# Performance work log

Measured on AMD Instinct MI355X. Metric: run time of the kernel, lower is better.

The kernel has to match this reference:

```python
import jax, jax.numpy as jnp
import numpy as np

N = 20000      # nodes
E = 300000     # edges
HID = 128
HEADS = 4
DH = HID // HEADS
NF = 4         # node_features
EF = 3         # edge_features
NS = 10        # num_servers (Q-head output)
NL = 4         # num_layers


def _ln(h, g, b):
    m = h.mean(-1, keepdims=True)
    v = ((h - m) ** 2).mean(-1, keepdims=True)
    return (h - m) / jnp.sqrt(v + 1e-5) * g + b


def _lrelu(h):
    return jnp.where(h >= 0, h, 0.2 * h)


def setup_inputs() -> dict:
    key = jax.random.key(0)
    ks = jax.random.split(key, 48)
    it = iter(range(48))

    def W(shape, fan_in):
        return jax.random.normal(ks[next(it)], shape, jnp.float32) / np.float32(np.sqrt(fan_in))

    inp = {}
    inp["x"] = jax.random.normal(ks[next(it)], (N, NF), jnp.float32)
    inp["edge_index"] = jax.random.randint(ks[next(it)], (2, E), 0, N)
    inp["edge_attr"] = jax.random.normal(ks[next(it)], (E, EF), jnp.float32)
    # node / edge encoders
    inp["ne_w"] = W((NF, HID), NF); inp["ne_b"] = jnp.zeros((HID,), jnp.float32)
    inp["ne_g"] = jnp.ones((HID,), jnp.float32); inp["ne_beta"] = jnp.zeros((HID,), jnp.float32)
    inp["ee_w"] = W((EF, HID), EF); inp["ee_b"] = jnp.zeros((HID,), jnp.float32)
    inp["ee_g"] = jnp.ones((HID,), jnp.float32); inp["ee_beta"] = jnp.zeros((HID,), jnp.float32)
    # EdgeConv layers (stacked over NL)
    inp["ec_w1"] = W((NL, 2 * HID, HID), 2 * HID); inp["ec_b1"] = jnp.zeros((NL, HID), jnp.float32)
    inp["ec_lng"] = jnp.ones((NL, HID), jnp.float32); inp["ec_lnb"] = jnp.zeros((NL, HID), jnp.float32)
    inp["ec_w2"] = W((NL, HID, HID), HID); inp["ec_b2"] = jnp.zeros((NL, HID), jnp.float32)
    inp["ec_wa"] = W((NL, 2 * HID, 1), 2 * HID); inp["ec_ba"] = jnp.zeros((NL, 1), jnp.float32)
    # GATConv layers
    inp["gat_w"] = W((NL, HID, HID), HID)
    inp["gat_asrc"] = W((NL, HEADS, DH), DH)
    inp["gat_adst"] = W((NL, HEADS, DH), DH)
    inp["gat_bias"] = jnp.zeros((NL, HID), jnp.float32)
    # post-block layer norms
    inp["ln_g"] = jnp.ones((NL, HID), jnp.float32); inp["ln_b"] = jnp.zeros((NL, HID), jnp.float32)
    # dueling heads
    inp["adv_w1"] = W((HID, HID), HID); inp["adv_b1"] = jnp.zeros((HID,), jnp.float32)
    inp["adv_g"] = jnp.ones((HID,), jnp.float32); inp["adv_beta"] = jnp.zeros((HID,), jnp.float32)
    inp["adv_w2"] = W((HID, NS), HID); inp["adv_b2"] = jnp.zeros((NS,), jnp.float32)
    inp["val_w1"] = W((HID, HID), HID); inp["val_b1"] = jnp.zeros((HID,), jnp.float32)
    inp["val_g"] = jnp.ones((HID,), jnp.float32); inp["val_beta"] = jnp.zeros((HID,), jnp.float32)
    inp["val_w2"] = W((HID, 1), HID); inp["val_b2"] = jnp.zeros((1,), jnp.float32)
    return inp


def _forward(x, edge_attr, edge_index,
             ne_w, ne_b, ne_g, ne_beta, ee_w, ee_b, ee_g, ee_beta,
             ec_w1, ec_b1, ec_lng, ec_lnb, ec_w2, ec_b2, ec_wa, ec_ba,
             gat_w, gat_asrc, gat_adst, gat_bias, ln_g, ln_b,
             adv_w1, adv_b1, adv_g, adv_beta, adv_w2, adv_b2,
             val_w1, val_b1, val_g, val_beta, val_w2, val_b2):
    src = edge_index[0]
    dst = edge_index[1]
    h = _ln(_lrelu(x @ ne_w + ne_b), ne_g, ne_beta)                 # node encoder (eval: no dropout)
    _ea = _ln(_lrelu(edge_attr @ ee_w + ee_b), ee_g, ee_beta)        # edge encoder; message() only tests presence
    deg = jax.ops.segment_sum(jnp.ones((E,), h.dtype), dst, num_segments=N)  # in-degree [N]
    sl = jnp.arange(N)
    src_sl = jnp.concatenate([src, sl])                              # GATConv adds self-loops
    dst_sl = jnp.concatenate([dst, sl])

    xc = h
    res = h
    for i in range(NL):
        # ---- EdgeConv: gather-concat, per-edge MLP, sigmoid edge-attention gate, scatter ----
        tmp = jnp.concatenate([xc[dst], xc[src]], axis=1)            # [E, 2H] = x_i || x_j
        m = _lrelu(tmp @ ec_w1[i] + ec_b1[i])
        m = _ln(m, ec_lng[i], ec_lnb[i])
        m = _lrelu(m @ ec_w2[i] + ec_b2[i])
        gate = jax.nn.sigmoid(tmp @ ec_wa[i] + ec_ba[i])             # [E, 1]
        msg = m * gate
        if i % 2 == 0:  # 'max' aggregation (PyG fills isolated nodes with 0)
            agg = jax.ops.segment_max(msg, dst, num_segments=N)
            agg = jnp.where(deg[:, None] > 0, agg, 0.0)
        else:           # 'mean'
            agg = jax.ops.segment_sum(msg, dst, num_segments=N) / jnp.maximum(deg, 1.0)[:, None]
        # ---- GATConv (self-loops, segment softmax over destination) ----
        wx = (xc @ gat_w[i]).reshape(N, HEADS, DH)
        asrc = (wx * gat_asrc[i]).sum(-1)                            # [N, HEADS]
        adst = (wx * gat_adst[i]).sum(-1)
        e = _lrelu(asrc[src_sl] + adst[dst_sl])                      # [E+N, HEADS]
        emax = jax.ops.segment_max(e, dst_sl, num_segments=N)
        p = jnp.exp(e - emax[dst_sl])
        den = jax.ops.segment_sum(p, dst_sl, num_segments=N)
        alpha = p / den[dst_sl]                                      # attention (eval: no dropout)
        gat_out = jax.ops.segment_sum(alpha[:, :, None] * wx[src_sl], dst_sl, num_segments=N)
        gat_out = gat_out.reshape(N, HID) + gat_bias[i]
        # ---- residual + norm + activation ----
        xc = _lrelu(_ln(res + agg + gat_out, ln_g[i], ln_b[i]))
        res = xc

    t = xc[0]                                                        # task node representation
    a = _ln(_lrelu(t @ adv_w1 + adv_b1), adv_g, adv_beta)
    a = a @ adv_w2 + adv_b2                                          # [NS]
    v = _ln(_lrelu(t @ val_w1 + val_b1), val_g, val_beta)
    v = v @ val_w2 + val_b2                                          # [1]
    q = v + (a - a.mean())
    return q, v


def reference(x, edge_index, edge_attr,
              ne_w, ne_b, ne_g, ne_beta, ee_w, ee_b, ee_g, ee_beta,
              ec_w1, ec_b1, ec_lng, ec_lnb, ec_w2, ec_b2, ec_wa, ec_ba,
              gat_w, gat_asrc, gat_adst, gat_bias, ln_g, ln_b,
              adv_w1, adv_b1, adv_g, adv_beta, adv_w2, adv_b2,
              val_w1, val_b1, val_g, val_beta, val_w2, val_b2):
    return _forward(x, edge_attr, edge_index,
                    ne_w, ne_b, ne_g, ne_beta, ee_w, ee_b, ee_g, ee_beta,
                    ec_w1, ec_b1, ec_lng, ec_lnb, ec_w2, ec_b2, ec_wa, ec_ba,
                    gat_w, gat_asrc, gat_adst, gat_bias, ln_g, ln_b,
                    adv_w1, adv_b1, adv_g, adv_beta, adv_w2, adv_b2,
                    val_w1, val_b1, val_g, val_beta, val_w2, val_b2)
```

## Files before the change

kernel.cpp:

```cpp
#include <hip/hip_runtime.h>
#include <hip/hip_bf16.h>

#define NN 20000
#define NE 300000
#define HIDN 128
#define NLAY 4
#define NNTILES ((NN + 63) / 64)
#define EBLOCKS64 4688
#define EB64_PER_XCD 586

typedef short short8 __attribute__((ext_vector_type(8)));
typedef float f32x4 __attribute__((ext_vector_type(4)));
typedef unsigned short us16;
typedef unsigned int u32;

__device__ __forceinline__ float lrelu(float x){ return x >= 0.f ? x : 0.2f * x; }
__device__ __forceinline__ float b2f(us16 u){ return __uint_as_float(((u32)u) << 16); }
__device__ __forceinline__ us16 f2b(float f){
    u32 u = __float_as_uint(f);
    u += 0x7FFFu + ((u >> 16) & 1u);
    return (us16)(u >> 16);
}
__device__ __forceinline__ float rawf(const void* p, size_t i, int dt){
    return dt ? b2f(((const us16*)p)[i]) : ((const float*)p)[i];
}
__device__ __forceinline__ void ld4f(const float* p, float* r){
    float4 v = *(const float4*)p; r[0]=v.x; r[1]=v.y; r[2]=v.z; r[3]=v.w;
}
__device__ __forceinline__ int swzi(int i){
    return (i & ~15) | ((i & 15) ^ (((i >> 5) & 3) << 2));
}

__device__ __forceinline__ void ln_stats_128(float v, volatile float* red, float& mean, float& inv){
    float s = v, s2 = v * v;
#pragma unroll
    for (int m = 32; m >= 1; m >>= 1){ s += __shfl_xor(s, m, 64); s2 += __shfl_xor(s2, m, 64); }
    int w = threadIdx.x >> 6;
    if ((threadIdx.x & 63) == 0){ red[w*2] = s; red[w*2+1] = s2; }
    __syncthreads();
    float ts = red[0] + red[2], ts2 = red[1] + red[3];
    mean = ts * (1.f/128.f);
    float var = ts2 * (1.f/128.f) - mean * mean;
    inv = rsqrtf(var + 1e-5f);
    __syncthreads();
}

__global__ void k_detect(const u32* __restrict__ ne_g, int* __restrict__ flag){
    flag[0] = (ne_g[0] == 0x3F803F80u) ? 1 : 0;
}

struct ConvEnt { const void* s; float* d; int n; int pad; };
struct ConvTab { ConvEnt c[28]; int cnt; int pad[3]; };

__global__ void k_convert_all(ConvTab tab, const int* __restrict__ flag){
    int ti = blockIdx.y;
    if (ti >= tab.cnt) return;
    const void* s = tab.c[ti].s;
    float* d = tab.c[ti].d;
    int n = tab.c[ti].n;
    int dt = flag[0];
    for (int i = blockIdx.x*blockDim.x + threadIdx.x; i < n; i += gridDim.x*blockDim.x)
        d[i] = rawf(s, i, dt);
}

#define W1T (128*256)
#define W2S (4*128*32)
#define GWT (128*128)
#define PER_L (W1T + W2S + GWT)
#define PTOT2 (NLAY*PER_L)
__global__ void k_prepw(const void* __restrict__ ecw1r, const void* __restrict__ ecw2r,
                        const void* __restrict__ gatwr, const int* __restrict__ flag,
                        us16* __restrict__ w1t, us16* __restrict__ w2s, us16* __restrict__ gwt){
    int id = blockIdx.x*blockDim.x + threadIdx.x;
    if (id >= PTOT2) return;
    int dt = flag[0];
    int L = id / PER_L, r = id % PER_L;
    if (r < W1T){
        int n = r >> 8, k = r & 255;
        w1t[(size_t)L*W1T + r] = f2b(rawf(ecw1r, (size_t)L*32768 + (size_t)k*128 + n, dt));
    } else if (r < W1T + W2S){
        int rr = r - W1T;
        int kk = rr >> 12, rem = rr & 4095, n = rem >> 5, ks = rem & 31;
        int k = kk*32 + ks;
        w2s[(size_t)L*W2S + rr] = f2b(rawf(ecw2r, (size_t)L*16384 + (size_t)k*128 + n, dt));
    } else {
        int rr = r - W1T - W2S; int n = rr >> 7, k = rr & 127;
        gwt[(size_t)L*GWT + rr] = f2b(rawf(gatwr, (size_t)L*16384 + (size_t)k*128 + n, dt));
    }
}

__global__ void k_hist(const int* __restrict__ dstI, int* __restrict__ cnt){
    int e = blockIdx.x*blockDim.x + threadIdx.x;
    if (e < NE) atomicAdd(&cnt[dstI[e]], 1);
}
__global__ void k_scan(const int* __restrict__ cnt, int* __restrict__ rowptr){
    __shared__ int ps[256];
    int t = threadIdx.x;
    int chunk = (NN + 255) / 256;
    int beg = t*chunk, end = beg + chunk; if (end > NN) end = NN;
    int s = 0;
    for (int i = beg; i < end; ++i) s += cnt[i];
    ps[t] = s; __syncthreads();
    int off = 0;
    for (int i = 0; i < t; ++i) off += ps[i];
    int run = off;
    for (int i = beg; i < end; ++i){ rowptr[i] = run; run += cnt[i]; }
    if (t == 255) rowptr[NN] = run;
}
__global__ void k_csrfill(const int* __restrict__ srcI, const int* __restrict__ dstI,
                          int* __restrict__ cur, int* __restrict__ csr_src,
                          int* __restrict__ csr_dst){
    int e = blockIdx.x*blockDim.x + threadIdx.x;
    if (e < NE){
        int d = dstI[e];
        int p = atomicAdd(&cur[d], 1);
        csr_src[p] = srcI[e];
        csr_dst[p] = d;
    }
}

__global__ void k_nodeenc(const float* __restrict__ xf, const float* __restrict__ w,
                          const float* __restrict__ b, const float* __restrict__ g,
                          const float* __restrict__ beta, float* __restrict__ h,
                          us16* __restrict__ xb){
    __shared__ float red[4];
    int n = blockIdx.x, t = threadIdx.x;
    float acc = b[t];
#pragma unroll
    for (int k = 0; k < 4; ++k) acc = fmaf(xf[n*4+k], w[k*HIDN+t], acc);
    acc = lrelu(acc);
    float mean, inv; ln_stats_128(acc, red, mean, inv);
    float o = (acc-mean)*inv*g[t] + beta[t];
    h[(size_t)n*HIDN+t] = o;
    xb[(size_t)n*HIDN+t] = f2b(o);
}

__global__ void k_predot(const float* __restrict__ x, const float* __restrict__ wa,
                         const float* __restrict__ baP, float* __restrict__ gd,
                         float* __restrict__ gs){
    int wv = threadIdx.x >> 6, l = threadIdx.x & 63;
    int n = blockIdx.x*4 + wv;
    if (n >= NN) return;
    float2 xv = *(const float2*)(x + (size_t)n*HIDN + 2*l);
    float pd = xv.x*wa[2*l]     + xv.y*wa[2*l+1];
    float ps = xv.x*wa[128+2*l] + xv.y*wa[129+2*l];
#pragma unroll
    for (int mk = 32; mk >= 1; mk >>= 1){ pd += __shfl_xor(pd, mk, 64); ps += __shfl_xor(ps, mk, 64); }
    if (l == 0){ gd[n] = pd + baP[0]; gs[n] = ps; }
}

__global__ __launch_bounds__(256, 2) void k_nodemm(
    const us16* __restrict__ xb, const us16* __restrict__ w1t,
    const us16* __restrict__ gwt, const float* __restrict__ b1,
    const float* __restrict__ aws, const float* __restrict__ awd,
    us16* __restrict__ y1b, us16* __restrict__ y2b, us16* __restrict__ wxb,
    float* __restrict__ asrc, float* __restrict__ adst)
{
    __shared__ __align__(16) us16 sbuf[64*128];
    int t = threadIdx.x;
    int wv = t >> 6, lane = t & 63, g = lane >> 4, lr = lane & 15;

    short8 fr[3][2][4];
#pragma unroll
    for (int m = 0; m < 3; ++m)
#pragma unroll
        for (int p = 0; p < 2; ++p){
            int crow = (wv + 4*p)*16 + lr;
#pragma unroll
            for (int kk = 0; kk < 4; ++kk){
                fr[m][p][kk] = (m < 2)
                    ? *(const short8*)(w1t + crow*256 + m*128 + kk*32 + g*8)
                    : *(const short8*)(gwt + crow*128 + kk*32 + g*8);
            }
        }
    float aw_s0 = aws[2*lane], aw_s1 = aws[2*lane+1];
    float aw_d0 = awd[2*lane], aw_d1 = awd[2*lane+1];
    float b1v[2][4];
#pragma unroll
    for (int p = 0; p < 2; ++p) ld4f(b1 + (wv + 4*p)*16 + g*4, b1v[p]);

    for (int tile = blockIdx.x; tile < NNTILES; tile += gridDim.x){
        int n0 = tile * 64;
        f32x4 acc[3][2][4];
#pragma unroll
        for (int m = 0; m < 3; ++m)
#pragma unroll
            for (int p = 0; p < 2; ++p)
#pragma unroll
                for (int et = 0; et < 4; ++et) acc[m][p][et] = (f32x4)(0.f);

#pragma unroll
        for (int et = 0; et < 4; ++et){
            int nrow = n0 + et*16 + lr; if (nrow >= NN) nrow = NN - 1;
            short8 bF[4];
#pragma unroll
            for (int kk = 0; kk < 4; ++kk)
                bF[kk] = *(const short8*)(xb + (size_t)nrow*HIDN + kk*32 + g*8);
#pragma unroll
            for (int m = 0; m < 3; ++m)
#pragma unroll
                for (int p = 0; p < 2; ++p)
#pragma unroll
                    for (int kk = 0; kk < 4; ++kk)
                        acc[m][p][et] = __builtin_amdgcn_mfma_f32_16x16x32_bf16(fr[m][p][kk], bF[kk], acc[m][p][et], 0, 0, 0);
        }

#pragma unroll
        for (int m = 0; m < 3; ++m){
#pragma unroll
            for (int p = 0; p < 2; ++p)
#pragma unroll
                for (int et = 0; et < 4; ++et){
                    int row = et*16 + lr;
                    int swz = (row & 7) << 3;
                    int c0 = (wv + 4*p)*16 + g*4;
#pragma unroll
                    for (int r = 0; r < 4; ++r){
                        float v = acc[m][p][et][r] + ((m == 0) ? b1v[p][r] : 0.f);
                        sbuf[row*128 + ((c0 + r) ^ swz)] = f2b(v);
                    }
                }
            __syncthreads();
            us16* dst = (m == 0) ? y1b : (m == 1) ? y2b : wxb;
            {
                int row = t >> 2, q = t & 3;
                int n = n0 + row;
                if (n < NN){
                    int swz = (row & 7) << 3;
#pragma unroll
                    for (int j = 0; j < 4; ++j){
                        int col = q*32 + j*8;
                        *(short8*)(dst + (size_t)n*HIDN + col) = *(const short8*)(sbuf + row*128 + (col ^ swz));
                    }
                }
            }
            if (m == 2){
#pragma unroll
                for (int i = 0; i < 16; ++i){
                    int rw = wv*16 + i;
                    int n2 = n0 + rw;
                    int ci = (2*lane) ^ ((rw & 7) << 3);
                    u32 v = *(const u32*)(sbuf + rw*128 + ci);
                    float x0 = b2f((us16)(v & 0xFFFFu)), x1 = b2f((us16)(v >> 16));
                    float ps = x0*aw_s0 + x1*aw_s1;
                    float pd = x0*aw_d0 + x1*aw_d1;
#pragma unroll
                    for (int mk = 8; mk >= 1; mk >>= 1){ ps += __shfl_xor(ps, mk, 64); pd += __shfl_xor(pd, mk, 64); }
                    if ((lane & 15) == 0 && n2 < NN){
                        int h = lane >> 4;
                        asrc[(size_t)n2*4 + h] = ps;
                        adst[(size_t)n2*4 + h] = pd;
                    }
                }
            }
            __syncthreads();
        }
    }
}

__global__ __launch_bounds__(256, 4) void k_edgeconv2(
    const us16* __restrict__ y1b, const us16* __restrict__ y2b,
    const int* __restrict__ csr_src, const int* __restrict__ csr_dst,
    const us16* __restrict__ w2s, const float* __restrict__ lngE,
    const float* __restrict__ lnbE, const float* __restrict__ b2,
    const float* __restrict__ gd, const float* __restrict__ gs,
    us16* __restrict__ msg)
{
    __shared__ __align__(16) u32 bsl[2][2048];
    __shared__ __align__(16) us16 outS[4*16*128];
    int t = threadIdx.x;
    int wv = t >> 6, lane = t & 63, g = lane >> 4, lr = lane & 15;
    int bid = (int)blockIdx.x;
    int sb = (bid & 7) * EB64_PER_XCD + (bid >> 3);
    int e0 = sb * 64;

    const u32* w2u = (const u32*)w2s;
    u32 rS[8];
#pragma unroll
    for (int q = 0; q < 8; ++q) rS[q] = w2u[t + 256*q];

    int e = e0 + wv*16 + lr;
    int ec = (e < NE) ? e : NE - 1;
    int d = csr_dst[ec], s = csr_src[ec];
    float gate = 1.f / (1.f + __expf(-(gd[d] + gs[s])));

    float vv[32];
    {
        short8 ra[4], rb[4];
#pragma unroll
        for (int kk = 0; kk < 4; ++kk){
            ra[kk] = *(const short8*)(y1b + (size_t)d*HIDN + kk*32 + g*8);
            rb[kk] = *(const short8*)(y2b + (size_t)s*HIDN + kk*32 + g*8);
        }
        float s1 = 0.f, s2 = 0.f;
#pragma unroll
        for (int kk = 0; kk < 4; ++kk)
#pragma unroll
            for (int j = 0; j < 8; ++j){
                float v = lrelu(b2f((us16)ra[kk][j]) + b2f((us16)rb[kk][j]));
                vv[kk*8+j] = v; s1 += v; s2 += v*v;
            }
        s1 += __shfl_xor(s1, 16, 64); s2 += __shfl_xor(s2, 16, 64);
        s1 += __shfl_xor(s1, 32, 64); s2 += __shfl_xor(s2, 32, 64);
        float mean = s1 * (1.f/128.f);
        float var  = s2 * (1.f/128.f) - mean*mean;
        float inv  = rsqrtf(var + 1e-5f);
#pragma unroll
        for (int kk = 0; kk < 4; ++kk){
            float lg[4], lg2[4], lb[4], lb2[4];
            int c0 = kk*32 + g*8;
            ld4f(lngE + c0, lg);  ld4f(lngE + c0 + 4, lg2);
            ld4f(lnbE + c0, lb);  ld4f(lnbE + c0 + 4, lb2);
#pragma unroll
            for (int j = 0; j < 4; ++j){
                vv[kk*8+j]   = (vv[kk*8+j]   - mean)*inv*lg[j]  + lb[j];
                vv[kk*8+4+j] = (vv[kk*8+4+j] - mean)*inv*lg2[j] + lb2[j];
            }
        }
    }
    short8 aF[4];
#pragma unroll
    for (int kk = 0; kk < 4; ++kk)
#pragma unroll
        for (int j = 0; j < 8; ++j)
            aF[kk][j] = (short)f2b(vv[kk*8+j]);

#pragma unroll
    for (int q = 0; q < 8; ++q) bsl[0][swzi(t + 256*q)] = rS[q];
#pragma unroll
    for (int q = 0; q < 8; ++q) rS[q] = w2u[2048 + t + 256*q];
    __syncthreads();

    f32x4 acc[8];
#pragma unroll
    for (int nt = 0; nt < 8; ++nt) acc[nt] = (f32x4)(0.f);
#pragma unroll
    for (int kk = 0; kk < 4; ++kk){
        const us16* bp = (const us16*)bsl[kk & 1];
#pragma unroll
        for (int nt = 0; nt < 8; ++nt){
            int row = nt*16 + lr;
            short8 bF = *(const short8*)(bp + row*32 + (g*8 ^ (((row>>1)&3)<<3)));
            acc[nt] = __builtin_amdgcn_mfma_f32_16x16x32_bf16(aF[kk], bF, acc[nt], 0, 0, 0);
        }
        if (kk < 3){
#pragma unroll
            for (int q = 0; q < 8; ++q) bsl[(kk+1)&1][swzi(t + 256*q)] = rS[q];
            if (kk < 2){
#pragma unroll
                for (int q = 0; q < 8; ++q) rS[q] = w2u[(kk+2)*2048 + t + 256*q];
            }
            __syncthreads();
        }
    }

    float b2v[8];
#pragma unroll
    for (int nt = 0; nt < 8; ++nt) b2v[nt] = b2[nt*16 + lr];
    us16* os = outS + wv*2048;
#pragma unroll
    for (int r = 0; r < 4; ++r){
        int i = g*4 + r;
        float gi = __shfl(gate, i, 64);
        int swz = (i & 7) << 3;
#pragma unroll
        for (int nt = 0; nt < 8; ++nt){
            float v = lrelu(acc[nt][r] + b2v[nt]) * gi;
            os[i*128 + ((nt*16 + lr) ^ swz)] = f2b(v);
        }
    }
    {
        int row = lane >> 2, q = lane & 3;
        int ew = e0 + wv*16 + row;
        if (ew < NE){
            int swz = (row & 7) << 3;
#pragma unroll
            for (int j = 0; j < 4; ++j){
                int col = q*32 + j*8;
                *(short8*)(msg + (size_t)ew*HIDN + col) = *(const short8*)(os + row*128 + (col ^ swz));
            }
        }
    }
}

__global__ __launch_bounds__(256, 8) void k_node_update(
    const int* __restrict__ rowptr, const int* __restrict__ csr_src,
    const us16* __restrict__ msg, const us16* __restrict__ wxb,
    const float* __restrict__ asrc, const float* __restrict__ adst,
    const float* __restrict__ xc, const float* __restrict__ gbias,
    const float* __restrict__ lng, const float* __restrict__ lnb,
    float* __restrict__ xout, us16* __restrict__ xbout, int maxmode)
{
    int wv = threadIdx.x >> 6, l = threadIdx.x & 63;
    int n = blockIdx.x*4 + wv;
    if (n >= NN) return;
    int c0 = 2*l, c1 = 2*l + 1;
    int h = l >> 4;

    int b = rowptr[n], en = rowptr[n+1];
    int deg = en - b;

    float adst_h = adst[(size_t)n*4 + h];
    float pself = __expf(fminf(lrelu(asrc[(size_t)n*4 + h] + adst_h), 80.f));
    u32 wq = *(const u32*)(wxb + (size_t)n*HIDN + c0);
    float att0 = pself * b2f((us16)(wq & 0xFFFFu));
    float att1 = pself * b2f((us16)(wq >> 16));
    float den = pself;

    float agg0, agg1;
    if (maxmode){ agg0 = agg1 = -3.0e38f; } else { agg0 = agg1 = 0.f; }

    for (int i = b; i < en; ++i){
        int s = csr_src[i];
        u32 mq = *(const u32*)(msg + (size_t)i*HIDN + c0);
        float m0 = b2f((us16)(mq & 0xFFFFu)), m1 = b2f((us16)(mq >> 16));
        if (maxmode){ agg0 = fmaxf(agg0, m0); agg1 = fmaxf(agg1, m1); }
        else        { agg0 += m0; agg1 += m1; }
        float p = __expf(fminf(lrelu(asrc[(size_t)s*4 + h] + adst_h), 80.f));
        u32 wq2 = *(const u32*)(wxb + (size_t)s*HIDN + c0);
        att0 = fmaf(p, b2f((us16)(wq2 & 0xFFFFu)), att0);
        att1 = fmaf(p, b2f((us16)(wq2 >> 16)), att1);
        den += p;
    }
    float rden = 1.f / den;
    att0 *= rden; att1 *= rden;
    if (maxmode){ if (deg == 0){ agg0 = 0.f; agg1 = 0.f; } }
    else { float rd = 1.f / fmaxf((float)deg, 1.f); agg0 *= rd; agg1 *= rd; }

    float2 xcv = *(const float2*)(xc + (size_t)n*HIDN + c0);
    float s0 = xcv.x + agg0 + att0 + gbias[c0];
    float s1 = xcv.y + agg1 + att1 + gbias[c1];

    float ss = s0 + s1, ss2 = s0*s0 + s1*s1;
#pragma unroll
    for (int mk = 32; mk >= 1; mk >>= 1){ ss += __shfl_xor(ss, mk, 64); ss2 += __shfl_xor(ss2, mk, 64); }
    float mean = ss * (1.f/128.f);
    float var  = ss2 * (1.f/128.f) - mean*mean;
    float inv  = rsqrtf(var + 1e-5f);
    float o0 = lrelu((s0-mean)*inv*lng[c0] + lnb[c0]);
    float o1 = lrelu((s1-mean)*inv*lng[c1] + lnb[c1]);
    *(float2*)(xout + (size_t)n*HIDN + c0) = make_float2(o0, o1);
    u32 pk = (u32)f2b(o0) | ((u32)f2b(o1) << 16);
    *(u32*)(xbout + (size_t)n*HIDN + c0) = pk;
}

__global__ void k_heads(const float* __restrict__ xc,
                        const float* __restrict__ aw1, const float* __restrict__ ab1,
                        const float* __restrict__ ag,  const float* __restrict__ abeta,
                        const float* __restrict__ aw2, const float* __restrict__ ab2,
                        const float* __restrict__ vw1, const float* __restrict__ vb1,
                        const float* __restrict__ vg,  const float* __restrict__ vbeta,
                        const float* __restrict__ vw2, const float* __restrict__ vb2,
                        void* __restrict__ dout, const int* __restrict__ flag){
    __shared__ float red[4];
    __shared__ float ts[128], u1[128], aout[10];
    int t = threadIdx.x;
    ts[t] = xc[t];
    __syncthreads();
    float acc = ab1[t];
    for (int k = 0; k < 128; ++k) acc = fmaf(ts[k], aw1[k*HIDN+t], acc);
    acc = lrelu(acc);
    float mean, inv; ln_stats_128(acc, red, mean, inv);
    u1[t] = (acc-mean)*inv*ag[t] + abeta[t];
    __syncthreads();
    if (t < 10){
        float a = ab2[t];
        for (int k = 0; k < 128; ++k) a = fmaf(u1[k], aw2[k*10+t], a);
        aout[t] = a;
    }
    __syncthreads();
    float accv = vb1[t];
    for (int k = 0; k < 128; ++k) accv = fmaf(ts[k], vw1[k*HIDN+t], accv);
    accv = lrelu(accv);
    float meanv, invv; ln_stats_128(accv, red, meanv, invv);
    float v1 = (accv-meanv)*invv*vg[t] + vbeta[t];
    float pv = v1 * vw2[t];
#pragma unroll
    for (int m = 32; m >= 1; m >>= 1) pv += __shfl_xor(pv, m, 64);
    if ((t & 63) == 0) red[t >> 6] = pv;
    __syncthreads();
    if (t == 0){
        float v = red[0] + red[1] + vb2[0];
        float am = 0.f;
        for (int j = 0; j < 10; ++j) am += aout[j];
        am *= 0.1f;
        int dt = flag[0];
        for (int j = 0; j < 11; ++j){
            float val = (j < 10) ? (v + aout[j] - am) : v;
            if (dt) ((__hip_bfloat16*)dout)[j] = __float2bfloat16(val);
            else    ((float*)dout)[j] = val;
        }
    }
}

extern "C" void kernel_launch(void* const* d_in, const int* in_sizes, int n_in,
                              void* d_out, int out_size, void* d_ws, size_t ws_size,
                              hipStream_t stream)
{
    float* base = (float*)d_ws;
    size_t off = 0;
    auto A = [&](size_t n)->float*{ float* p = base + off; off += (n + 63) & ~(size_t)63; return p; };

    int*   flag   = (int*)A(64);
    float* xf     = A((size_t)NN*4);
    float* new_w  = A(4*HIDN); float* neb = A(HIDN); float* neg_ = A(HIDN); float* nebeta = A(HIDN);
    float* ecb1   = A(NLAY*HIDN);
    float* eclng  = A(NLAY*HIDN); float* eclnb = A(NLAY*HIDN);
    float* ecb2   = A(NLAY*HIDN);
    float* ecwa   = A(NLAY*256);  float* ecba = A(NLAY);
    float* gasrc  = A(NLAY*HIDN); float* gadst = A(NLAY*HIDN); float* gbias = A(NLAY*HIDN);
    float* lng    = A(NLAY*HIDN); float* lnb = A(NLAY*HIDN);
    float* aw1    = A(HIDN*HIDN); float* ab1 = A(HIDN); float* ag = A(HIDN); float* abeta = A(HIDN);
    float* aw2    = A(HIDN*10);   float* ab2 = A(10);
    float* vw1    = A(HIDN*HIDN); float* vb1 = A(HIDN); float* vg = A(HIDN); float* vbeta = A(HIDN);
    float* vw2    = A(HIDN);      float* vb2 = A(1);
    us16* w1t = (us16*)A((size_t)NLAY*W1T/2);
    us16* w2s = (us16*)A((size_t)NLAY*W2S/2);
    us16* gwt = (us16*)A((size_t)NLAY*GWT/2);
    us16* xb   = (us16*)A((size_t)NN*HIDN/2);
    us16* wxb  = (us16*)A((size_t)NN*HIDN/2);
    us16* y1b  = (us16*)A((size_t)NN*HIDN/2);
    us16* y2b  = (us16*)A((size_t)NN*HIDN/2);
    float* xcA = A((size_t)NN*HIDN);
    float* xcB = A((size_t)NN*HIDN);
    float* gd  = A(NN); float* gs = A(NN);
    int* cnt     = (int*)A(NN);
    int* rowptr  = (int*)A(NN+1);
    int* cur     = (int*)A(NN);
    int* csr_src = (int*)A(NE);
    int* csr_dst = (int*)A(NE);
    float* asrc = A(NN*4); float* adst = A(NN*4);
    us16* msg = (us16*)A((size_t)NE*HIDN/2);

    const int* ei   = (const int*)d_in[1];
    const int* srcI = ei;
    const int* dstI = ei + NE;

    k_detect<<<1, 1, 0, stream>>>((const u32*)d_in[5], flag);

    ConvTab tab; int cc = 0;
    auto add = [&](int idx, float* dst, int n){ tab.c[cc].s = d_in[idx]; tab.c[cc].d = dst; tab.c[cc].n = n; tab.c[cc].pad = 0; cc++; };
    add(0,  xf,    NN*4);
    add(3,  new_w, 4*HIDN); add(4, neb, HIDN); add(5, neg_, HIDN); add(6, nebeta, HIDN);
    add(12, ecb1, NLAY*HIDN);
    add(13, eclng, NLAY*HIDN);     add(14, eclnb, NLAY*HIDN);
    add(16, ecb2, NLAY*HIDN);
    add(17, ecwa, NLAY*256);       add(18, ecba, NLAY);
    add(20, gasrc, NLAY*HIDN); add(21, gadst, NLAY*HIDN); add(22, gbias, NLAY*HIDN);
    add(23, lng,   NLAY*HIDN); add(24, lnb, NLAY*HIDN);
    add(25, aw1, HIDN*HIDN); add(26, ab1, HIDN); add(27, ag, HIDN); add(28, abeta, HIDN);
    add(29, aw2, HIDN*10);   add(30, ab2, 10);
    add(31, vw1, HIDN*HIDN); add(32, vb1, HIDN); add(33, vg, HIDN); add(34, vbeta, HIDN);
    add(35, vw2, HIDN);      add(36, vb2, 1);
    tab.cnt = cc;
    dim3 cgrid(64, cc);
    k_convert_all<<<cgrid, 256, 0, stream>>>(tab, flag);

    k_prepw<<<(PTOT2+255)/256, 256, 0, stream>>>(d_in[11], d_in[15], d_in[19],
                                                 flag, w1t, w2s, gwt);

    hipMemsetAsync(cnt, 0, NN*sizeof(int), stream);
    k_hist<<<(NE+255)/256, 256, 0, stream>>>(dstI, cnt);
    k_scan<<<1, 256, 0, stream>>>(cnt, rowptr);
    hipMemcpyAsync(cur, rowptr, NN*sizeof(int), hipMemcpyDeviceToDevice, stream);
    k_csrfill<<<(NE+255)/256, 256, 0, stream>>>(srcI, dstI, cur, csr_src, csr_dst);

    k_nodeenc<<<NN, 128, 0, stream>>>(xf, new_w, neb, neg_, nebeta, xcA, xb);

    float* curx = xcA; float* nxt = xcB;
    int nblocks4 = (NN + 3) / 4;
    for (int i = 0; i < NLAY; ++i){
        int maxmode = (i % 2 == 0);

        k_predot<<<nblocks4, 256, 0, stream>>>(curx, ecwa + i*256, ecba + i, gd, gs);

        k_nodemm<<<NNTILES, 256, 0, stream>>>(xb, w1t + (size_t)i*W1T,
            gwt + (size_t)i*GWT, ecb1 + i*HIDN,
            gasrc + i*HIDN, gadst + i*HIDN,
            y1b, y2b, wxb, asrc, adst);

        k_edgeconv2<<<EBLOCKS64, 256, 0, stream>>>(y1b, y2b, csr_src, csr_dst,
            w2s + (size_t)i*W2S, eclng + i*HIDN, eclnb + i*HIDN,
            ecb2 + i*HIDN, gd, gs, msg);

        k_node_update<<<nblocks4, 256, 0, stream>>>(rowptr, csr_src, msg, wxb,
            asrc, adst, curx, gbias + i*HIDN, lng + i*HIDN, lnb + i*HIDN,
            nxt, xb, maxmode);

        float* tswap = curx; curx = nxt; nxt = tswap;
    }

    k_heads<<<1, 128, 0, stream>>>(curx, aw1, ab1, ag, abeta, aw2, ab2,
                                   vw1, vb1, vg, vbeta, vw2, vb2, d_out, flag);
}
```

Before: 591.8 us.

## Fuse attention pre-dot into node GEMM, shrink node tiles, prefetch CSR source index

Removes the separate k_predot launch per layer and computes the edge-attention gd/gs dot products inside k_nodemm from the bf16 node features already loaded for the MFMA. The node tile is halved from 64 to 32 rows, doubling the grid for more parallelism at the cost of reloading weights in more blocks. The node-update gather loop prefetches the next csr_src index and issues the asrc/wxb loads earlier to hide latency. The fused dot product uses bf16-rounded features instead of the fp32 ones, which slightly changes precision.

```diff
diff --git a/kernel.cpp b/kernel.cpp
--- a/kernel.cpp
+++ b/kernel.cpp
@@ -5,7 +5,7 @@
 #define NE 300000
 #define HIDN 128
 #define NLAY 4
-#define NNTILES ((NN + 63) / 64)
+#define NNT32 ((NN + 31) / 32)
 #define EBLOCKS64 4688
 #define EB64_PER_XCD 586
 
@@ -135,28 +135,16 @@
     xb[(size_t)n*HIDN+t] = f2b(o);
 }
 
-__global__ void k_predot(const float* __restrict__ x, const float* __restrict__ wa,
-                         const float* __restrict__ baP, float* __restrict__ gd,
-                         float* __restrict__ gs){
-    int wv = threadIdx.x >> 6, l = threadIdx.x & 63;
-    int n = blockIdx.x*4 + wv;
-    if (n >= NN) return;
-    float2 xv = *(const float2*)(x + (size_t)n*HIDN + 2*l);
-    float pd = xv.x*wa[2*l]     + xv.y*wa[2*l+1];
-    float ps = xv.x*wa[128+2*l] + xv.y*wa[129+2*l];
-#pragma unroll
-    for (int mk = 32; mk >= 1; mk >>= 1){ pd += __shfl_xor(pd, mk, 64); ps += __shfl_xor(ps, mk, 64); }
-    if (l == 0){ gd[n] = pd + baP[0]; gs[n] = ps; }
-}
-
 __global__ __launch_bounds__(256, 2) void k_nodemm(
     const us16* __restrict__ xb, const us16* __restrict__ w1t,
     const us16* __restrict__ gwt, const float* __restrict__ b1,
     const float* __restrict__ aws, const float* __restrict__ awd,
+    const float* __restrict__ wa, const float* __restrict__ baP,
     us16* __restrict__ y1b, us16* __restrict__ y2b, us16* __restrict__ wxb,
-    float* __restrict__ asrc, float* __restrict__ adst)
+    float* __restrict__ asrc, float* __restrict__ adst,
+    float* __restrict__ gd, float* __restrict__ gs)
 {
-    __shared__ __align__(16) us16 sbuf[64*128];
+    __shared__ __align__(16) us16 sbuf[32*128];
     int t = threadIdx.x;
     int wv = t >> 6, lane = t & 63, g = lane >> 4, lr = lane & 15;
 
@@ -178,19 +166,27 @@
     float b1v[2][4];
 #pragma unroll
     for (int p = 0; p < 2; ++p) ld4f(b1 + (wv + 4*p)*16 + g*4, b1v[p]);
-
-    for (int tile = blockIdx.x; tile < NNTILES; tile += gridDim.x){
-        int n0 = tile * 64;
-        f32x4 acc[3][2][4];
+    float wadv[4][8], wasv[4][8];
+#pragma unroll
+    for (int kk = 0; kk < 4; ++kk){
+        int c0 = kk*32 + g*8;
+        ld4f(wa + c0, &wadv[kk][0]);        ld4f(wa + c0 + 4, &wadv[kk][4]);
+        ld4f(wa + 128 + c0, &wasv[kk][0]);  ld4f(wa + 128 + c0 + 4, &wasv[kk][4]);
+    }
+    float ba = baP[0];
+
+    for (int tile = blockIdx.x; tile < NNT32; tile += gridDim.x){
+        int n0 = tile * 32;
+        f32x4 acc[3][2][2];
 #pragma unroll
         for (int m = 0; m < 3; ++m)
 #pragma unroll
             for (int p = 0; p < 2; ++p)
 #pragma unroll
-                for (int et = 0; et < 4; ++et) acc[m][p][et] = (f32x4)(0.f);
-
-#pragma unroll
-        for (int et = 0; et < 4; ++et){
+                for (int et = 0; et < 2; ++et) acc[m][p][et] = (f32x4)(0.f);
+
+#pragma unroll
+        for (int et = 0; et < 2; ++et){
             int nrow = n0 + et*16 + lr; if (nrow >= NN) nrow = NN - 1;
             short8 bF[4];
 #pragma unroll
@@ -203,6 +199,21 @@
 #pragma unroll
                     for (int kk = 0; kk < 4; ++kk)
                         acc[m][p][et] = __builtin_amdgcn_mfma_f32_16x16x32_bf16(fr[m][p][kk], bF[kk], acc[m][p][et], 0, 0, 0);
+            if (wv == 0){
+                float pd = 0.f, ps = 0.f;
+#pragma unroll
+                for (int kk = 0; kk < 4; ++kk)
+#pragma unroll
+                    for (int j = 0; j < 8; ++j){
+                        float xv = b2f((us16)bF[kk][j]);
+                        pd = fmaf(xv, wadv[kk][j], pd);
+                        ps = fmaf(xv, wasv[kk][j], ps);
+                    }
+                pd += __shfl_xor(pd, 16, 64); ps += __shfl_xor(ps, 16, 64);
+                pd += __shfl_xor(pd, 32, 64); ps += __shfl_xor(ps, 32, 64);
+                int n2 = n0 + et*16 + lr;
+                if (g == 0 && n2 < NN){ gd[n2] = pd + ba; gs[n2] = ps; }
+            }
         }
 
 #pragma unroll
@@ -210,7 +221,7 @@
 #pragma unroll
             for (int p = 0; p < 2; ++p)
 #pragma unroll
-                for (int et = 0; et < 4; ++et){
+                for (int et = 0; et < 2; ++et){
                     int row = et*16 + lr;
                     int swz = (row & 7) << 3;
                     int c0 = (wv + 4*p)*16 + g*4;
@@ -223,21 +234,21 @@
             __syncthreads();
             us16* dst = (m == 0) ? y1b : (m == 1) ? y2b : wxb;
             {
-                int row = t >> 2, q = t & 3;
+                int row = t >> 3, q = t & 7;
                 int n = n0 + row;
                 if (n < NN){
                     int swz = (row & 7) << 3;
 #pragma unroll
-                    for (int j = 0; j < 4; ++j){
-                        int col = q*32 + j*8;
+                    for (int j = 0; j < 2; ++j){
+                        int col = q*16 + j*8;
                         *(short8*)(dst + (size_t)n*HIDN + col) = *(const short8*)(sbuf + row*128 + (col ^ swz));
                     }
                 }
             }
             if (m == 2){
 #pragma unroll
-                for (int i = 0; i < 16; ++i){
-                    int rw = wv*16 + i;
+                for (int i = 0; i < 8; ++i){
+                    int rw = wv*8 + i;
                     int n2 = n0 + rw;
                     int ci = (2*lane) ^ ((rw & 7) << 3);
                     u32 v = *(const u32*)(sbuf + rw*128 + ci);
@@ -410,14 +421,17 @@
     float agg0, agg1;
     if (maxmode){ agg0 = agg1 = -3.0e38f; } else { agg0 = agg1 = 0.f; }
 
+    int s_cur = (deg > 0) ? csr_src[b] : 0;
     for (int i = b; i < en; ++i){
-        int s = csr_src[i];
+        int s = s_cur;
+        if (i + 1 < en) s_cur = csr_src[i + 1];
         u32 mq = *(const u32*)(msg + (size_t)i*HIDN + c0);
+        float asr = asrc[(size_t)s*4 + h];
+        u32 wq2 = *(const u32*)(wxb + (size_t)s*HIDN + c0);
         float m0 = b2f((us16)(mq & 0xFFFFu)), m1 = b2f((us16)(mq >> 16));
         if (maxmode){ agg0 = fmaxf(agg0, m0); agg1 = fmaxf(agg1, m1); }
         else        { agg0 += m0; agg1 += m1; }
-        float p = __expf(fminf(lrelu(asrc[(size_t)s*4 + h] + adst_h), 80.f));
-        u32 wq2 = *(const u32*)(wxb + (size_t)s*HIDN + c0);
+        float p = __expf(fminf(lrelu(asr + adst_h), 80.f));
         att0 = fmaf(p, b2f((us16)(wq2 & 0xFFFFu)), att0);
         att1 = fmaf(p, b2f((us16)(wq2 >> 16)), att1);
         den += p;
@@ -572,12 +586,11 @@
     for (int i = 0; i < NLAY; ++i){
         int maxmode = (i % 2 == 0);
 
-        k_predot<<<nblocks4, 256, 0, stream>>>(curx, ecwa + i*256, ecba + i, gd, gs);
-
-        k_nodemm<<<NNTILES, 256, 0, stream>>>(xb, w1t + (size_t)i*W1T,
+        k_nodemm<<<NNT32, 256, 0, stream>>>(xb, w1t + (size_t)i*W1T,
             gwt + (size_t)i*GWT, ecb1 + i*HIDN,
             gasrc + i*HIDN, gadst + i*HIDN,
-            y1b, y2b, wxb, asrc, adst);
+            ecwa + i*256, ecba + i,
+            y1b, y2b, wxb, asrc, adst, gd, gs);
 
         k_edgeconv2<<<EBLOCKS64, 256, 0, stream>>>(y1b, y2b, csr_src, csr_dst,
             w2s + (size_t)i*W2S, eclng + i*HIDN, eclnb + i*HIDN,
```

New measurement: 570.3 us. -3.6%, faster.
